# Kernel tuning notes

Measured on AMD Instinct MI355X. Metric: run time of the kernel, lower is better.

## Reference

```python
import jax, jax.numpy as jnp
import numpy as np

N, E, F = 50000, 400000, 32

_WN = ["w10","w11","w20","w21","w30","w31","w40","w41","wl01","wl02","wl1","wl2"]
_BN = ["b10","b11","b20","b21","b30","b31","b40","b41","bl01","bl02","bl1","bl2"]
_DIMS = [(4,F),(F,F),(2*F+F+4,F),(F,F),(6*F,F),(F,F),(6*F,F),(F,F),(F,F),(F,F),(F,4),(F,1)]


def _lin(key, fin, fout):
    kw, kb = jax.random.split(key)
    w = jax.random.normal(kw, (fin, fout), jnp.float32) / np.float32(np.sqrt(fin))
    b = jax.random.normal(kb, (fout,), jnp.float32) * 0.01
    return w, b


def setup_inputs() -> dict:
    key = jax.random.key(0)
    ks = jax.random.split(key, 5)
    inp = {}
    inp["x"] = jax.random.normal(ks[0], (N, 4), jnp.float32)
    inp["edge_index"] = jax.random.randint(ks[1], (2, E), 0, N, jnp.int32)
    inp["edge_attr"] = jax.random.normal(ks[2], (E, 4), jnp.float32)
    inp["beta"] = jax.random.normal(ks[3], (N, 3), jnp.float32)
    lkeys = jax.random.split(ks[4], len(_DIMS))
    for i, (fin, fout) in enumerate(_DIMS):
        w, b = _lin(lkeys[i], fin, fout)
        inp[_WN[i]] = w
        inp[_BN[i]] = b
    return inp


def reference(x, edge_index, edge_attr, beta,
              w10, b10, w11, b11, w20, b20, w21, b21,
              w30, b30, w31, b31, w40, b40, w41, b41,
              wl01, bl01, wl02, bl02, wl1, bl1, wl2, bl2):
    row, col = edge_index[0], edge_index[1]
    n = x.shape[0]

    def mlp2(m, w0, b0, w1, b1):
        return jax.nn.relu(m @ w0 + b0) @ w1 + b1

    def seg_mean(h):  # scatter-mean onto target nodes (row), dim_size=n
        s = jax.ops.segment_sum(h, row, num_segments=n)
        c = jax.ops.segment_sum(jnp.ones((h.shape[0], 1), h.dtype), row, num_segments=n)
        return s / jnp.maximum(c, 1.0)

    # conv1: x is zeros with dim 4 (<=5), so message = mlp0(edge_attr)
    e1 = mlp2(edge_attr, w10, b10, w11, b11)            # [E,32]
    x1 = jax.nn.relu(seg_mean(e1)); e1 = jax.nn.relu(e1)
    # conv2
    ea2 = jnp.concatenate([edge_attr, e1], axis=1)      # [E,36]
    e2 = mlp2(jnp.concatenate([x1[row], x1[col], ea2], axis=1), w20, b20, w21, b21)
    x2 = jax.nn.relu(seg_mean(e2)); e2 = jax.nn.relu(e2)
    # conv3
    x21 = jnp.concatenate([x2, x1], axis=1)             # [N,64]
    ea3 = jnp.concatenate([e2, e1], axis=1)             # [E,64]
    e3 = mlp2(jnp.concatenate([x21[row], x21[col], ea3], axis=1), w30, b30, w31, b31)
    x3 = jax.nn.relu(seg_mean(e3)); e3 = jax.nn.relu(e3)
    # conv4 (node aggregate x4 is never used downstream, so skipped)
    x32 = jnp.concatenate([x3, x2], axis=1)
    ea4 = jnp.concatenate([e3, e2], axis=1)
    e4 = jax.nn.relu(mlp2(jnp.concatenate([x32[row], x32[col], ea4], axis=1), w40, b40, w41, b41))
    # heads
    out01 = e4 @ wl01 + bl01
    out02 = e4 @ wl02 + bl02
    edge_x = out01 @ wl1 + bl1 + edge_attr
    edge_x = edge_x / jnp.maximum(jnp.linalg.norm(edge_x, axis=1, keepdims=True), 1e-12)
    probs = jax.nn.sigmoid(out02 @ wl2 + bl2)           # [E,1]
    return (probs, edge_x, beta)
```

## Files before the change

### kernel.cpp

```cpp
#include <hip/hip_runtime.h>
#include <hip/hip_bf16.h>

#define EE 400000
#define NN 50000
#define SCAN_NBLK ((NN + 1023) / 1024)
#define NTILES (EE / 16)
#define TPX (NTILES / 8)
#define NPTILES ((NN + 15) / 16)

typedef float f32x4 __attribute__((ext_vector_type(4)));
typedef __bf16 bf16x8 __attribute__((ext_vector_type(8)));
typedef unsigned int u32;

static __device__ __forceinline__ bf16x8 u4_as_bf8(uint4 u) {
  return __builtin_bit_cast(bf16x8, u);
}
static __device__ __forceinline__ u32 relu_pk2(u32 d) {
  u32 m = (d & 0x80008000u) >> 15;
  m ^= 0x00010001u;
  return d & ((m << 16) - m);
}
static __device__ __forceinline__ u32 pk2bf(float a, float b) {
  union { __bf16 h[2]; u32 w; } t;
  t.h[0] = (__bf16)a; t.h[1] = (__bf16)b;
  return t.w;
}

__global__ void init_kernel(int* __restrict__ deg,
                            const float* __restrict__ bl01, const float* __restrict__ bl02,
                            const float* __restrict__ wl1,  const float* __restrict__ bl1,
                            const float* __restrict__ wl2,  const float* __restrict__ bl2,
                            float* __restrict__ headw) {
  int i = blockIdx.x * blockDim.x + threadIdx.x;
  if (i < NN) deg[i] = 0;
  if (blockIdx.x == 0) {
    int t = threadIdx.x;
    if (t < 4) {
      float s = bl1[t];
      for (int j = 0; j < 32; ++j) s += bl01[j] * wl1[j * 4 + t];
      headw[160 + t] = s;
    } else if (t == 4) {
      float s = bl2[0];
      for (int j = 0; j < 32; ++j) s += bl02[j] * wl2[j];
      headw[164] = s;
    }
  }
}

__global__ void pack_all_kernel(const float* __restrict__ w10, const float* __restrict__ w11,
                                const float* __restrict__ w20, const float* __restrict__ w21,
                                const float* __restrict__ w30, const float* __restrict__ w31,
                                const float* __restrict__ w40, const float* __restrict__ w41,
                                const float* __restrict__ wl01, const float* __restrict__ wl1,
                                const float* __restrict__ wl02, const float* __restrict__ wl2,
                                __bf16* __restrict__ pk) {
  const int f = blockIdx.x;
  const int t = threadIdx.x;
  int stage, lf;
  const float *W0, *W1;
  if (f < 4)       { stage = 1; lf = f;      W0 = w10; W1 = w11; }
  else if (f < 14) { stage = 2; lf = f - 4;  W0 = w20; W1 = w21; }
  else if (f < 28) { stage = 3; lf = f - 14; W0 = w30; W1 = w31; }
  else             { stage = 4; lf = f - 28; W0 = w40; W1 = w41; }
#pragma unroll
  for (int u = 0; u < 2; ++u) {
    int idx = t * 2 + u;
    int lane = idx >> 3, i = idx & 7;
    int l15 = lane & 15, g = lane >> 4;
    int k = 8 * g + i;
    float v = 0.f;
    if (stage == 1) {
      if (lf < 2)      v = (k < 4) ? W0[k * 32 + lf * 16 + l15] : 0.f;
      else             v = W1[k * 32 + (lf - 2) * 16 + l15];
    } else if (stage == 2) {
      if (lf < 4)      { int part = lf >> 1, nb = lf & 1; v = W0[(part * 32 + k) * 32 + nb * 16 + l15]; }
      else if (lf < 6) { int nb = lf - 4; v = (k < 4) ? W0[(64 + k) * 32 + nb * 16 + l15] : 0.f; }
      else if (lf < 8) { int nb = lf - 6; v = W0[(68 + k) * 32 + nb * 16 + l15]; }
      else             { int nb = lf - 8; v = W1[k * 32 + nb * 16 + l15]; }
    } else {
      if (lf < 8)       { int part = lf >> 2, kb = (lf >> 1) & 1, nb = lf & 1;
                          v = W0[(part * 64 + kb * 32 + k) * 32 + nb * 16 + l15]; }
      else if (lf < 12) { int eb = (lf - 8) >> 1, nb = lf & 1;
                          v = W0[(128 + eb * 32 + k) * 32 + nb * 16 + l15]; }
      else if (lf < 14) { int nb = lf - 12; v = W1[k * 32 + nb * 16 + l15]; }
      else {
        if (l15 < 4)      { float s = 0.f; for (int j = 0; j < 32; ++j) s += wl01[k * 32 + j] * wl1[j * 4 + l15]; v = s; }
        else if (l15 == 4){ float s = 0.f; for (int j = 0; j < 32; ++j) s += wl02[k * 32 + j] * wl2[j]; v = s; }
      }
    }
    pk[f * 512 + idx] = (__bf16)v;
  }
}

__global__ void hist_kernel(const int* __restrict__ rowi, int* __restrict__ deg) {
  int e = blockIdx.x * blockDim.x + threadIdx.x;
  if (e < EE) atomicAdd(&deg[rowi[e]], 1);
}

__global__ void scanA_kernel(const int* __restrict__ deg, int* __restrict__ offs,
                             int* __restrict__ partial) {
  __shared__ int lds[1024];
  const int t = threadIdx.x;
  const int i = blockIdx.x * 1024 + t;
  int v = (i < NN) ? deg[i] : 0;
  lds[t] = v;
  __syncthreads();
  for (int off = 1; off < 1024; off <<= 1) {
    int u = (t >= off) ? lds[t - off] : 0;
    __syncthreads();
    lds[t] += u;
    __syncthreads();
  }
  int incl = lds[t];
  if (i < NN) offs[i] = incl - v;
  if (t == 1023) partial[blockIdx.x] = incl;
}

__global__ void scanB_kernel(const int* __restrict__ partial, int* __restrict__ offs,
                             int* __restrict__ cursor) {
  __shared__ int sbase;
  const int t = threadIdx.x;
  const int b = blockIdx.x;
  if (t < 64) {
    int s = (t < b && t < SCAN_NBLK) ? partial[t] : 0;
#pragma unroll
    for (int o = 32; o > 0; o >>= 1) s += __shfl_down(s, o);
    if (t == 0) sbase = s;
  }
  __syncthreads();
  const int base = sbase;
  const int i = b * 1024 + t;
  if (i < NN) {
    int o = offs[i] + base;
    offs[i] = o;
    cursor[i] = o;
  }
  if (b == 0 && t == 0) offs[NN] = EE;
}

__global__ void scatter_kernel(const int* __restrict__ rowi, const int* __restrict__ coli,
                               const float* __restrict__ eattr, int* __restrict__ cursor,
                               int* __restrict__ rows_s, int* __restrict__ cols_s,
                               __bf16* __restrict__ ebf, float* __restrict__ eattr_s,
                               int* __restrict__ inv) {
  int e = blockIdx.x * blockDim.x + threadIdx.x;
  if (e >= EE) return;
  int r = rowi[e];
  int p = atomicAdd(&cursor[r], 1);
  inv[e] = p;
  rows_s[p] = r;
  cols_s[p] = coli[e];
  const float4 v = *(const float4*)(eattr + (size_t)e * 4);
  *(float4*)(eattr_s + (size_t)p * 4) = v;
  *(uint2*)(ebf + (size_t)p * 4) = make_uint2(pk2bf(v.x, v.y), pk2bf(v.z, v.w));
}

__global__ void agg_kernel(const __bf16* __restrict__ esrc,
                           const int* __restrict__ offs,
                           __bf16* __restrict__ dst1, int s1, int o1,
                           __bf16* __restrict__ dst2, int s2, int o2) {
  int idx = blockIdx.x * blockDim.x + threadIdx.x;
  int n = idx >> 5;
  int j = idx & 31;
  if (n >= NN) return;
  int a = offs[n], b = offs[n + 1];
  float s = 0.f;
  for (int t = a; t < b; ++t)
    s += (float)esrc[(size_t)t * 32 + j];
  float mean = s / fmaxf((float)(b - a), 1.f);
  __bf16 x = (__bf16)fmaxf(mean, 0.f);
  dst1[(size_t)n * s1 + o1 + j] = x;
  if (dst2) dst2[(size_t)n * s2 + o2 + j] = x;
}

template <int NPK>
__launch_bounds__(256, 4)
__global__ void nodeproj_kernel(const __bf16* __restrict__ pk,
                                const __bf16* __restrict__ xcat, int xoff, int xstride,
                                __bf16* __restrict__ ub) {
  constexpr int NKB = NPK / 32;
  const int tid = threadIdx.x;
  const int lane = tid & 63;
  const int wid = tid >> 6;
  const int l15 = lane & 15;
  const int g = lane >> 4;

  bf16x8 Br[NKB][2], Bc[NKB][2];
#pragma unroll
  for (int kb = 0; kb < NKB; ++kb)
#pragma unroll
    for (int nb = 0; nb < 2; ++nb) {
      Br[kb][nb] = *(const bf16x8*)(pk + (size_t)((0 * NKB + kb) * 2 + nb) * 512 + lane * 8);
      Bc[kb][nb] = *(const bf16x8*)(pk + (size_t)((1 * NKB + kb) * 2 + nb) * 512 + lane * 8);
    }

  const int t = blockIdx.x * 4 + wid;
  if (t >= NPTILES) return;
  const int base = t * 16;
  const int n = base + l15;
  const int nc = (n < NN) ? n : (NN - 1);

  f32x4 r0 = {0,0,0,0}, r1 = {0,0,0,0}, c0 = {0,0,0,0}, c1 = {0,0,0,0};
#pragma unroll
  for (int kb = 0; kb < NKB; ++kb) {
    bf16x8 a = *(const bf16x8*)(xcat + (size_t)nc * xstride + xoff + kb * 32 + 8 * g);
    r0 = __builtin_amdgcn_mfma_f32_16x16x32_bf16(a, Br[kb][0], r0, 0, 0, 0);
    r1 = __builtin_amdgcn_mfma_f32_16x16x32_bf16(a, Br[kb][1], r1, 0, 0, 0);
    c0 = __builtin_amdgcn_mfma_f32_16x16x32_bf16(a, Bc[kb][0], c0, 0, 0, 0);
    c1 = __builtin_amdgcn_mfma_f32_16x16x32_bf16(a, Bc[kb][1], c1, 0, 0, 0);
  }
#pragma unroll
  for (int r = 0; r < 4; ++r) {
    int m = 4 * g + r;
    if (base + m < NN) {
      size_t row = (size_t)(base + m) * 64;
      ub[row + l15]      = (__bf16)r0[r];
      ub[row + 16 + l15] = (__bf16)r1[r];
      ub[row + 32 + l15] = (__bf16)c0[r];
      ub[row + 48 + l15] = (__bf16)c1[r];
    }
  }
}

template <int STAGE>
__launch_bounds__(256, 5)
__global__ void conv_kernel(const __bf16* __restrict__ pk,
                            const float* __restrict__ B0, const float* __restrict__ B1v,
                            const int* __restrict__ rows_s, const int* __restrict__ cols_s,
                            const __bf16* __restrict__ ebf,
                            const __bf16* __restrict__ ub,
                            const __bf16* __restrict__ ein1,
                            const __bf16* __restrict__ ein2,
                            __bf16* __restrict__ d1,
                            const float* __restrict__ eattr_s,
                            const float* __restrict__ headw,
                            float* __restrict__ tmpP, float* __restrict__ tmpEX) {
  constexpr int NEB  = (STAGE == 1) ? 1 : 2;
  constexpr int FEB  = (STAGE == 1) ? 0 : (STAGE == 2) ? 4 : 8;
  constexpr int FW1  = (STAGE == 1) ? 2 : (STAGE == 2) ? 8 : 12;
  __shared__ __align__(16) float ldsH[4 * 16 * 36];

  const int tid = threadIdx.x;
  const int lane = tid & 63;
  const int wid = tid >> 6;
  const int l15 = lane & 15;
  const int g = lane >> 4;

  bf16x8 Bf[NEB][2];
#pragma unroll
  for (int eb = 0; eb < NEB; ++eb)
#pragma unroll
    for (int nb = 0; nb < 2; ++nb)
      Bf[eb][nb] = *(const bf16x8*)(pk + (size_t)(FEB + eb * 2 + nb) * 512 + lane * 8);
  bf16x8 B2f[2];
#pragma unroll
  for (int nb = 0; nb < 2; ++nb)
    B2f[nb] = *(const bf16x8*)(pk + (size_t)(FW1 + nb) * 512 + lane * 8);

  bf16x8 I0, I1;
#pragma unroll
  for (int i = 0; i < 8; ++i) {
    int k = 8 * g + i;
    I0[i] = (k == l15)      ? (__bf16)1.0f : (__bf16)0.0f;
    I1[i] = (k == 16 + l15) ? (__bf16)1.0f : (__bf16)0.0f;
  }

  const float b0j0 = B0[l15], b0j1 = B0[l15 + 16];
  const float b1j0 = B1v[l15], b1j1 = B1v[l15 + 16];

  bf16x8 Bh;
  float bexc = 0.f, bp = 0.f;
  if (STAGE == 4) {
    Bh = *(const bf16x8*)(pk + (size_t)14 * 512 + lane * 8);
    if (l15 < 4) bexc = headw[160 + l15];
    bp = headw[164];
  }

  float* hl = &ldsH[wid * 576];

  const int xcd = blockIdx.x & 7;
  const int wloc = (blockIdx.x >> 3) * 4 + wid;
  const int nwl = (gridDim.x >> 3) * 4;
  for (int t0 = wloc; t0 < TPX; t0 += nwl) {
    const int t = xcd * TPX + t0;
    const int base = t * 16;
    const int p = base + l15;

    bf16x8 urf, ucf;
    if (STAGE >= 2) {
      int rid = rows_s[p], cid = cols_s[p];
      urf = *(const bf16x8*)(ub + (size_t)rid * 64 + 8 * g);
      ucf = *(const bf16x8*)(ub + (size_t)cid * 64 + 32 + 8 * g);
    }

    bf16x8 ae;
    if (STAGE <= 2) {
      uint4 u = {0, 0, 0, 0};
      if (g == 0) {
        const uint2 v = *(const uint2*)(ebf + (size_t)p * 4);
        u.x = v.x; u.y = v.y;
      }
      ae = u4_as_bf8(u);
    }

    f32x4 a0a = {0,0,0,0}, a0b = {0,0,0,0}, a1a = {0,0,0,0}, a1b = {0,0,0,0};
    if (STAGE >= 2) {
      a0a = __builtin_amdgcn_mfma_f32_16x16x32_bf16(urf, I0, a0a, 0, 0, 0);
      a1a = __builtin_amdgcn_mfma_f32_16x16x32_bf16(urf, I1, a1a, 0, 0, 0);
      a0a = __builtin_amdgcn_mfma_f32_16x16x32_bf16(ucf, I0, a0a, 0, 0, 0);
      a1a = __builtin_amdgcn_mfma_f32_16x16x32_bf16(ucf, I1, a1a, 0, 0, 0);
    }
#pragma unroll
    for (int eb = 0; eb < NEB; ++eb) {
      bf16x8 a;
      if (STAGE == 1) {
        a = ae;
      } else if (STAGE == 2) {
        if (eb == 0) a = ae;
        else {
          uint4 u = *(const uint4*)(ein1 + (size_t)p * 32 + 8 * g);
          u.x = relu_pk2(u.x); u.y = relu_pk2(u.y); u.z = relu_pk2(u.z); u.w = relu_pk2(u.w);
          a = u4_as_bf8(u);
        }
      } else {
        const __bf16* src = (eb == 0) ? ein1 : ein2;
        uint4 u = *(const uint4*)(src + (size_t)p * 32 + 8 * g);
        u.x = relu_pk2(u.x); u.y = relu_pk2(u.y); u.z = relu_pk2(u.z); u.w = relu_pk2(u.w);
        a = u4_as_bf8(u);
      }
      a0b = __builtin_amdgcn_mfma_f32_16x16x32_bf16(a, Bf[eb][0], a0b, 0, 0, 0);
      a1b = __builtin_amdgcn_mfma_f32_16x16x32_bf16(a, Bf[eb][1], a1b, 0, 0, 0);
    }
    f32x4 acc0 = a0a + a0b, acc1 = a1a + a1b;

#pragma unroll
    for (int r = 0; r < 4; ++r) {
      int m = 4 * g + r;
      hl[m * 36 + l15]      = fmaxf(acc0[r] + b0j0, 0.f);
      hl[m * 36 + l15 + 16] = fmaxf(acc1[r] + b0j1, 0.f);
    }
    f32x4 h0 = *(const f32x4*)&hl[l15 * 36 + 8 * g];
    f32x4 h1 = *(const f32x4*)&hl[l15 * 36 + 8 * g + 4];
    bf16x8 a2;
#pragma unroll
    for (int i = 0; i < 4; ++i) { a2[i] = (__bf16)h0[i]; a2[i + 4] = (__bf16)h1[i]; }
    f32x4 o0 = {0,0,0,0}, o1 = {0,0,0,0};
    o0 = __builtin_amdgcn_mfma_f32_16x16x32_bf16(a2, B2f[0], o0, 0, 0, 0);
    o1 = __builtin_amdgcn_mfma_f32_16x16x32_bf16(a2, B2f[1], o1, 0, 0, 0);

    if (STAGE <= 3) {
#pragma unroll
      for (int r = 0; r < 4; ++r) {
        int m = 4 * g + r;
        size_t eo = (size_t)(base + m) * 32;
        d1[eo + l15]      = (__bf16)(o0[r] + b1j0);
        d1[eo + l15 + 16] = (__bf16)(o1[r] + b1j1);
      }
    } else {
#pragma unroll
      for (int r = 0; r < 4; ++r) {
        int m = 4 * g + r;
        hl[m * 36 + l15]      = fmaxf(o0[r] + b1j0, 0.f);
        hl[m * 36 + l15 + 16] = fmaxf(o1[r] + b1j1, 0.f);
      }
      f32x4 q0 = *(const f32x4*)&hl[l15 * 36 + 8 * g];
      f32x4 q1 = *(const f32x4*)&hl[l15 * 36 + 8 * g + 4];
      bf16x8 a3;
#pragma unroll
      for (int i = 0; i < 4; ++i) { a3[i] = (__bf16)q0[i]; a3[i + 4] = (__bf16)q1[i]; }
      f32x4 ho = {0,0,0,0};
      ho = __builtin_amdgcn_mfma_f32_16x16x32_bf16(a3, Bh, ho, 0, 0, 0);
#pragma unroll
      for (int r = 0; r < 4; ++r) {
        int m = 4 * g + r;
        int po = base + m;
        float s = ho[r];
        float v = 0.f, sq = 0.f;
        if (l15 < 4) {
          v = s + bexc + eattr_s[(size_t)po * 4 + l15];
          sq = v * v;
        }
        sq += __shfl_xor(sq, 1);
        sq += __shfl_xor(sq, 2);
        if (l15 < 4) tmpEX[(size_t)po * 4 + l15] = v * (1.f / fmaxf(sqrtf(sq), 1e-12f));
        if (l15 == 4) tmpP[po] = 1.f / (1.f + __expf(-(s + bp)));
      }
    }
  }
}

__global__ void unpermute_kernel(const int* __restrict__ inv,
                                 const float* __restrict__ tmpP,
                                 const float* __restrict__ tmpEX,
                                 const float* __restrict__ beta,
                                 float* __restrict__ outP, float* __restrict__ outEX,
                                 float* __restrict__ outB) {
  int e = blockIdx.x * blockDim.x + threadIdx.x;
  if (e >= EE) return;
  int p = inv[e];
  outP[e] = tmpP[p];
  float4 ex = *(const float4*)(tmpEX + (size_t)p * 4);
  *(float4*)(outEX + (size_t)e * 4) = ex;
  if (e < NN * 3) outB[e] = beta[e];
}

extern "C" void kernel_launch(void* const* d_in, const int* in_sizes, int n_in,
                              void* d_out, int out_size, void* d_ws, size_t ws_size,
                              hipStream_t stream) {
  const float* eattr = (const float*)d_in[2];
  const float* beta = (const float*)d_in[3];
  const float* w10 = (const float*)d_in[4];  const float* b10 = (const float*)d_in[5];
  const float* w11 = (const float*)d_in[6];  const float* b11 = (const float*)d_in[7];
  const float* w20 = (const float*)d_in[8];  const float* b20 = (const float*)d_in[9];
  const float* w21 = (const float*)d_in[10]; const float* b21 = (const float*)d_in[11];
  const float* w30 = (const float*)d_in[12]; const float* b30 = (const float*)d_in[13];
  const float* w31 = (const float*)d_in[14]; const float* b31 = (const float*)d_in[15];
  const float* w40 = (const float*)d_in[16]; const float* b40 = (const float*)d_in[17];
  const float* w41 = (const float*)d_in[18]; const float* b41 = (const float*)d_in[19];
  const float* wl01 = (const float*)d_in[20]; const float* bl01 = (const float*)d_in[21];
  const float* wl02 = (const float*)d_in[22]; const float* bl02 = (const float*)d_in[23];
  const float* wl1 = (const float*)d_in[24];  const float* bl1 = (const float*)d_in[25];
  const float* wl2 = (const float*)d_in[26];  const float* bl2 = (const float*)d_in[27];
  const int* rowi = (const int*)d_in[1];
  const int* coli = rowi + EE;

  char* w = (char*)d_ws;
  auto alloc = [&](size_t bytes) {
    char* p = w;
    w += (bytes + 255) & ~(size_t)255;
    return p;
  };
  __bf16* e1b = (__bf16*)alloc((size_t)EE * 32 * 2);
  __bf16* e2b = (__bf16*)alloc((size_t)EE * 32 * 2);
  __bf16* e3b = (__bf16*)alloc((size_t)EE * 32 * 2);
  __bf16* ub  = (__bf16*)alloc((size_t)NN * 64 * 2);
  __bf16* x21 = (__bf16*)alloc((size_t)NN * 64 * 2);
  __bf16* x32 = (__bf16*)alloc((size_t)NN * 64 * 2);
  int* deg = (int*)alloc(NN * 4);
  int* offs = (int*)alloc((NN + 1) * 4);
  int* cursor = (int*)alloc(NN * 4);
  int* rows_s = (int*)alloc(EE * 4);
  int* cols_s = (int*)alloc(EE * 4);
  int* inv = (int*)alloc(EE * 4);
  __bf16* ebf = (__bf16*)alloc((size_t)EE * 4 * 2);
  float* eattr_s = (float*)alloc((size_t)EE * 4 * 4);
  float* tmpP = (float*)alloc((size_t)EE * 4);
  float* tmpEX = (float*)alloc((size_t)EE * 4 * 4);
  float* headw = (float*)alloc(256 * 4);
  int* partial = (int*)alloc(64 * 4);
  __bf16* packw = (__bf16*)alloc((size_t)43 * 512 * 2);

  float* outP = (float*)d_out;
  float* outEX = outP + EE;
  float* outB = outP + (size_t)5 * EE;

  __bf16* pk1 = packw;
  __bf16* pk2 = packw + 4 * 512;
  __bf16* pk3 = packw + 14 * 512;
  __bf16* pk4 = packw + 28 * 512;

  init_kernel<<<(NN + 255) / 256, 256, 0, stream>>>(deg, bl01, bl02, wl1, bl1, wl2, bl2, headw);
  pack_all_kernel<<<43, 256, 0, stream>>>(w10, w11, w20, w21, w30, w31, w40, w41,
                                          wl01, wl1, wl02, wl2, packw);
  hist_kernel<<<(EE + 255) / 256, 256, 0, stream>>>(rowi, deg);
  scanA_kernel<<<SCAN_NBLK, 1024, 0, stream>>>(deg, offs, partial);
  scanB_kernel<<<SCAN_NBLK, 1024, 0, stream>>>(partial, offs, cursor);
  scatter_kernel<<<(EE + 255) / 256, 256, 0, stream>>>(rowi, coli, eattr, cursor,
                                                       rows_s, cols_s, ebf, eattr_s, inv);

  conv_kernel<1><<<2048, 256, 0, stream>>>(pk1, b10, b11, rows_s, cols_s, ebf,
                                           (const __bf16*)nullptr, (const __bf16*)nullptr,
                                           (const __bf16*)nullptr, e1b,
                                           (const float*)nullptr, (const float*)nullptr,
                                           (float*)nullptr, (float*)nullptr);
  agg_kernel<<<(NN * 32 + 255) / 256, 256, 0, stream>>>(e1b, offs, x21, 64, 32,
                                                        (__bf16*)nullptr, 0, 0);
  nodeproj_kernel<32><<<(NPTILES + 3) / 4, 256, 0, stream>>>(pk2, x21, 32, 64, ub);
  conv_kernel<2><<<2048, 256, 0, stream>>>(pk2, b20, b21, rows_s, cols_s, ebf,
                                           ub, e1b, (const __bf16*)nullptr, e2b,
                                           (const float*)nullptr, (const float*)nullptr,
                                           (float*)nullptr, (float*)nullptr);
  agg_kernel<<<(NN * 32 + 255) / 256, 256, 0, stream>>>(e2b, offs, x21, 64, 0, x32, 64, 32);
  nodeproj_kernel<64><<<(NPTILES + 3) / 4, 256, 0, stream>>>(pk3, x21, 0, 64, ub);
  conv_kernel<3><<<2048, 256, 0, stream>>>(pk3, b30, b31, rows_s, cols_s, ebf,
                                           ub, e2b, e1b, e3b,
                                           (const float*)nullptr, (const float*)nullptr,
                                           (float*)nullptr, (float*)nullptr);
  agg_kernel<<<(NN * 32 + 255) / 256, 256, 0, stream>>>(e3b, offs, x32, 64, 0,
                                                        (__bf16*)nullptr, 0, 0);
  nodeproj_kernel<64><<<(NPTILES + 3) / 4, 256, 0, stream>>>(pk4, x32, 0, 64, ub);
  conv_kernel<4><<<2048, 256, 0, stream>>>(pk4, b40, b41, rows_s, cols_s, ebf,
                                           ub, e3b, e2b, (__bf16*)nullptr,
                                           eattr_s, headw, tmpP, tmpEX);
  unpermute_kernel<<<(EE + 255) / 256, 256, 0, stream>>>(inv, tmpP, tmpEX, beta,
                                                         outP, outEX, outB);
}
```

Before: 228.0 us.

## Chunk the counting sort into eight segments and pack per-edge data into records

Splits the edge histogram and scatter into 8 contiguous edge chunks, each with its own per-node counters and offsets, so atomics spread over 8x more counters. Agg now walks 8 segments per node. Row index, column index and bf16 edge attributes are packed into one 16-byte record per sorted edge, so each conv lane does a single vector load instead of several separate arrays. The stage-4 residual now uses bf16 edge attributes from the record instead of fp32, which loses some precision. Edges are sorted chunk-major, which weakens row locality for gathers and segment sums.

Result: slower. 239.5 us (+5.0%).

```diff
diff --git a/kernel.cpp b/kernel.cpp
--- a/kernel.cpp
+++ b/kernel.cpp
@@ -3,7 +3,10 @@
 
 #define EE 400000
 #define NN 50000
-#define SCAN_NBLK ((NN + 1023) / 1024)
+#define NCH 8
+#define CHUNK (EE / NCH)
+#define NTOT (NCH * NN)
+#define SCAN_NBLK ((NTOT + 1023) / 1024)
 #define NTILES (EE / 16)
 #define TPX (NTILES / 8)
 #define NPTILES ((NN + 15) / 16)
@@ -26,13 +29,13 @@
   return t.w;
 }
 
-__global__ void init_kernel(int* __restrict__ deg,
+__global__ void init_kernel(int* __restrict__ count,
                             const float* __restrict__ bl01, const float* __restrict__ bl02,
                             const float* __restrict__ wl1,  const float* __restrict__ bl1,
                             const float* __restrict__ wl2,  const float* __restrict__ bl2,
                             float* __restrict__ headw) {
   int i = blockIdx.x * blockDim.x + threadIdx.x;
-  if (i < NN) deg[i] = 0;
+  if (i < NTOT) count[i] = 0;
   if (blockIdx.x == 0) {
     int t = threadIdx.x;
     if (t < 4) {
@@ -92,17 +95,22 @@
   }
 }
 
-__global__ void hist_kernel(const int* __restrict__ rowi, int* __restrict__ deg) {
-  int e = blockIdx.x * blockDim.x + threadIdx.x;
-  if (e < EE) atomicAdd(&deg[rowi[e]], 1);
-}
-
-__global__ void scanA_kernel(const int* __restrict__ deg, int* __restrict__ offs,
+__global__ void hist_kernel(const int* __restrict__ rowi, int* __restrict__ count) {
+  const int c = blockIdx.x & 7;
+  const int lb = blockIdx.x >> 3;
+  const int nb = gridDim.x >> 3;
+  for (int i = lb * blockDim.x + threadIdx.x; i < CHUNK; i += nb * blockDim.x) {
+    int e = c * CHUNK + i;
+    atomicAdd(&count[c * NN + rowi[e]], 1);
+  }
+}
+
+__global__ void scanA_kernel(const int* __restrict__ count, int* __restrict__ offs,
                              int* __restrict__ partial) {
   __shared__ int lds[1024];
   const int t = threadIdx.x;
   const int i = blockIdx.x * 1024 + t;
-  int v = (i < NN) ? deg[i] : 0;
+  int v = (i < NTOT) ? count[i] : 0;
   lds[t] = v;
   __syncthreads();
   for (int off = 1; off < 1024; off <<= 1) {
@@ -112,7 +120,7 @@
     __syncthreads();
   }
   int incl = lds[t];
-  if (i < NN) offs[i] = incl - v;
+  if (i < NTOT) offs[i] = incl - v;
   if (t == 1023) partial[blockIdx.x] = incl;
 }
 
@@ -122,7 +130,8 @@
   const int t = threadIdx.x;
   const int b = blockIdx.x;
   if (t < 64) {
-    int s = (t < b && t < SCAN_NBLK) ? partial[t] : 0;
+    int s = 0;
+    for (int j = t; j < b; j += 64) s += partial[j];
 #pragma unroll
     for (int o = 32; o > 0; o >>= 1) s += __shfl_down(s, o);
     if (t == 0) sbase = s;
@@ -130,29 +139,33 @@
   __syncthreads();
   const int base = sbase;
   const int i = b * 1024 + t;
-  if (i < NN) {
+  if (i < NTOT) {
     int o = offs[i] + base;
     offs[i] = o;
     cursor[i] = o;
   }
-  if (b == 0 && t == 0) offs[NN] = EE;
+  if (b == 0 && t == 0) offs[NTOT] = EE;
 }
 
 __global__ void scatter_kernel(const int* __restrict__ rowi, const int* __restrict__ coli,
                                const float* __restrict__ eattr, int* __restrict__ cursor,
-                               int* __restrict__ rows_s, int* __restrict__ cols_s,
-                               __bf16* __restrict__ ebf, float* __restrict__ eattr_s,
-                               int* __restrict__ inv) {
-  int e = blockIdx.x * blockDim.x + threadIdx.x;
-  if (e >= EE) return;
-  int r = rowi[e];
-  int p = atomicAdd(&cursor[r], 1);
-  inv[e] = p;
-  rows_s[p] = r;
-  cols_s[p] = coli[e];
-  const float4 v = *(const float4*)(eattr + (size_t)e * 4);
-  *(float4*)(eattr_s + (size_t)p * 4) = v;
-  *(uint2*)(ebf + (size_t)p * 4) = make_uint2(pk2bf(v.x, v.y), pk2bf(v.z, v.w));
+                               uint4* __restrict__ record, int* __restrict__ inv) {
+  const int c = blockIdx.x & 7;
+  const int lb = blockIdx.x >> 3;
+  const int nb = gridDim.x >> 3;
+  for (int i = lb * blockDim.x + threadIdx.x; i < CHUNK; i += nb * blockDim.x) {
+    int e = c * CHUNK + i;
+    int r = rowi[e];
+    int p = atomicAdd(&cursor[c * NN + r], 1);
+    inv[e] = p;
+    const float4 v = *(const float4*)(eattr + (size_t)e * 4);
+    uint4 rec;
+    rec.x = (u32)r;
+    rec.y = (u32)coli[e];
+    rec.z = pk2bf(v.x, v.y);
+    rec.w = pk2bf(v.z, v.w);
+    record[p] = rec;
+  }
 }
 
 __global__ void agg_kernel(const __bf16* __restrict__ esrc,
@@ -163,11 +176,16 @@
   int n = idx >> 5;
   int j = idx & 31;
   if (n >= NN) return;
-  int a = offs[n], b = offs[n + 1];
   float s = 0.f;
-  for (int t = a; t < b; ++t)
-    s += (float)esrc[(size_t)t * 32 + j];
-  float mean = s / fmaxf((float)(b - a), 1.f);
+  int cnt = 0;
+#pragma unroll
+  for (int c = 0; c < NCH; ++c) {
+    int a = offs[c * NN + n], b = offs[c * NN + n + 1];
+    cnt += b - a;
+    for (int t = a; t < b; ++t)
+      s += (float)esrc[(size_t)t * 32 + j];
+  }
+  float mean = s / fmaxf((float)cnt, 1.f);
   __bf16 x = (__bf16)fmaxf(mean, 0.f);
   dst1[(size_t)n * s1 + o1 + j] = x;
   if (dst2) dst2[(size_t)n * s2 + o2 + j] = x;
@@ -226,13 +244,11 @@
 __launch_bounds__(256, 5)
 __global__ void conv_kernel(const __bf16* __restrict__ pk,
                             const float* __restrict__ B0, const float* __restrict__ B1v,
-                            const int* __restrict__ rows_s, const int* __restrict__ cols_s,
-                            const __bf16* __restrict__ ebf,
+                            const uint4* __restrict__ record,
                             const __bf16* __restrict__ ub,
                             const __bf16* __restrict__ ein1,
                             const __bf16* __restrict__ ein2,
                             __bf16* __restrict__ d1,
-                            const float* __restrict__ eattr_s,
                             const float* __restrict__ headw,
                             float* __restrict__ tmpP, float* __restrict__ tmpEX) {
   constexpr int NEB  = (STAGE == 1) ? 1 : 2;
@@ -286,9 +302,11 @@
     const int base = t * 16;
     const int p = base + l15;
 
+    const uint4 rec = record[p];
+
     bf16x8 urf, ucf;
     if (STAGE >= 2) {
-      int rid = rows_s[p], cid = cols_s[p];
+      int rid = (int)rec.x, cid = (int)rec.y;
       urf = *(const bf16x8*)(ub + (size_t)rid * 64 + 8 * g);
       ucf = *(const bf16x8*)(ub + (size_t)cid * 64 + 32 + 8 * g);
     }
@@ -296,10 +314,7 @@
     bf16x8 ae;
     if (STAGE <= 2) {
       uint4 u = {0, 0, 0, 0};
-      if (g == 0) {
-        const uint2 v = *(const uint2*)(ebf + (size_t)p * 4);
-        u.x = v.x; u.y = v.y;
-      }
+      if (g == 0) { u.x = rec.z; u.y = rec.w; }
       ae = u4_as_bf8(u);
     }
 
@@ -375,9 +390,13 @@
         int m = 4 * g + r;
         int po = base + m;
         float s = ho[r];
+        u32 zz = __shfl(rec.z, m);
+        u32 ww = __shfl(rec.w, m);
         float v = 0.f, sq = 0.f;
         if (l15 < 4) {
-          v = s + bexc + eattr_s[(size_t)po * 4 + l15];
+          u32 wzw = (l15 & 2) ? ww : zz;
+          u32 bits = (l15 & 1) ? (wzw & 0xffff0000u) : (wzw << 16);
+          v = s + bexc + __uint_as_float(bits);
           sq = v * v;
         }
         sq += __shfl_xor(sq, 1);
@@ -436,18 +455,15 @@
   __bf16* ub  = (__bf16*)alloc((size_t)NN * 64 * 2);
   __bf16* x21 = (__bf16*)alloc((size_t)NN * 64 * 2);
   __bf16* x32 = (__bf16*)alloc((size_t)NN * 64 * 2);
-  int* deg = (int*)alloc(NN * 4);
-  int* offs = (int*)alloc((NN + 1) * 4);
-  int* cursor = (int*)alloc(NN * 4);
-  int* rows_s = (int*)alloc(EE * 4);
-  int* cols_s = (int*)alloc(EE * 4);
+  int* count = (int*)alloc(NTOT * 4);
+  int* offs = (int*)alloc((NTOT + 1) * 4);
+  int* cursor = (int*)alloc(NTOT * 4);
   int* inv = (int*)alloc(EE * 4);
-  __bf16* ebf = (__bf16*)alloc((size_t)EE * 4 * 2);
-  float* eattr_s = (float*)alloc((size_t)EE * 4 * 4);
+  uint4* record = (uint4*)alloc((size_t)EE * 16);
   float* tmpP = (float*)alloc((size_t)EE * 4);
   float* tmpEX = (float*)alloc((size_t)EE * 4 * 4);
   float* headw = (float*)alloc(256 * 4);
-  int* partial = (int*)alloc(64 * 4);
+  int* partial = (int*)alloc(512 * 4);
   __bf16* packw = (__bf16*)alloc((size_t)43 * 512 * 2);
 
   float* outP = (float*)d_out;
@@ -459,39 +475,35 @@
   __bf16* pk3 = packw + 14 * 512;
   __bf16* pk4 = packw + 28 * 512;
 
-  init_kernel<<<(NN + 255) / 256, 256, 0, stream>>>(deg, bl01, bl02, wl1, bl1, wl2, bl2, headw);
+  init_kernel<<<(NTOT + 255) / 256, 256, 0, stream>>>(count, bl01, bl02, wl1, bl1, wl2, bl2, headw);
   pack_all_kernel<<<43, 256, 0, stream>>>(w10, w11, w20, w21, w30, w31, w40, w41,
                                           wl01, wl1, wl02, wl2, packw);
-  hist_kernel<<<(EE + 255) / 256, 256, 0, stream>>>(rowi, deg);
-  scanA_kernel<<<SCAN_NBLK, 1024, 0, stream>>>(deg, offs, partial);
+  hist_kernel<<<1024, 256, 0, stream>>>(rowi, count);
+  scanA_kernel<<<SCAN_NBLK, 1024, 0, stream>>>(count, offs, partial);
   scanB_kernel<<<SCAN_NBLK, 1024, 0, stream>>>(partial, offs, cursor);
-  scatter_kernel<<<(EE + 255) / 256, 256, 0, stream>>>(rowi, coli, eattr, cursor,
-                                                       rows_s, cols_s, ebf, eattr_s, inv);
-
-  conv_kernel<1><<<2048, 256, 0, stream>>>(pk1, b10, b11, rows_s, cols_s, ebf,
+  scatter_kernel<<<1024, 256, 0, stream>>>(rowi, coli, eattr, cursor, record, inv);
+
+  conv_kernel<1><<<2048, 256, 0, stream>>>(pk1, b10, b11, record,
                                            (const __bf16*)nullptr, (const __bf16*)nullptr,
                                            (const __bf16*)nullptr, e1b,
-                                           (const float*)nullptr, (const float*)nullptr,
-                                           (float*)nullptr, (float*)nullptr);
+                                           (const float*)nullptr, (float*)nullptr, (float*)nullptr);
   agg_kernel<<<(NN * 32 + 255) / 256, 256, 0, stream>>>(e1b, offs, x21, 64, 32,
                                                         (__bf16*)nullptr, 0, 0);
   nodeproj_kernel<32><<<(NPTILES + 3) / 4, 256, 0, stream>>>(pk2, x21, 32, 64, ub);
-  conv_kernel<2><<<2048, 256, 0, stream>>>(pk2, b20, b21, rows_s, cols_s, ebf,
+  conv_kernel<2><<<2048, 256, 0, stream>>>(pk2, b20, b21, record,
                                            ub, e1b, (const __bf16*)nullptr, e2b,
-                                           (const float*)nullptr, (const float*)nullptr,
-                                           (float*)nullptr, (float*)nullptr);
+                                           (const float*)nullptr, (float*)nullptr, (float*)nullptr);
   agg_kernel<<<(NN * 32 + 255) / 256, 256, 0, stream>>>(e2b, offs, x21, 64, 0, x32, 64, 32);
   nodeproj_kernel<64><<<(NPTILES + 3) / 4, 256, 0, stream>>>(pk3, x21, 0, 64, ub);
-  conv_kernel<3><<<2048, 256, 0, stream>>>(pk3, b30, b31, rows_s, cols_s, ebf,
+  conv_kernel<3><<<2048, 256, 0, stream>>>(pk3, b30, b31, record,
                                            ub, e2b, e1b, e3b,
-                                           (const float*)nullptr, (const float*)nullptr,
-                                           (float*)nullptr, (float*)nullptr);
+                                           (const float*)nullptr, (float*)nullptr, (float*)nullptr);
   agg_kernel<<<(NN * 32 + 255) / 256, 256, 0, stream>>>(e3b, offs, x32, 64, 0,
                                                         (__bf16*)nullptr, 0, 0);
   nodeproj_kernel<64><<<(NPTILES + 3) / 4, 256, 0, stream>>>(pk4, x32, 0, 64, ub);
-  conv_kernel<4><<<2048, 256, 0, stream>>>(pk4, b40, b41, rows_s, cols_s, ebf,
+  conv_kernel<4><<<2048, 256, 0, stream>>>(pk4, b40, b41, record,
                                            ub, e3b, e2b, (__bf16*)nullptr,
-                                           eattr_s, headw, tmpP, tmpEX);
+                                           headw, tmpP, tmpEX);
   unpermute_kernel<<<(EE + 255) / 256, 256, 0, stream>>>(inv, tmpP, tmpEX, beta,
                                                          outP, outEX, outB);
 }
```
